# Performance work log

Hardware: AMD Instinct MI355X
Metric: run time of the kernel (lower is better)

Reference implementation:

```python
import jax, jax.numpy as jnp
import numpy as np

N_NODES = 100000


def sage_conv(x, src, dst, w_self, w_neigh, b):
    # DGL SAGEConv with 'mean' aggregator: out = x @ W_self + mean_neigh(x) @ W_neigh + b
    msg = x[src]                                                     # [E, d] gather
    agg = jax.ops.segment_sum(msg, dst, num_segments=N_NODES)        # [N, d]
    deg = jax.ops.segment_sum(jnp.ones((src.shape[0],), x.dtype), dst,
                              num_segments=N_NODES)                  # [N]
    h_neigh = agg / jnp.maximum(deg, 1.0)[:, None]                   # mean; 0 for isolated nodes
    return x @ w_self + h_neigh @ w_neigh + b


def setup_inputs() -> dict:
    key = jax.random.key(0)
    ks = jax.random.split(key, 12)
    N, E = N_NODES, 1600000
    in_f, h_f, r_f = 128, 128, 64
    glorot = lambda k, i, o: jax.random.normal(k, (i, o), jnp.float32) / np.float32(np.sqrt(i))
    return {
        "in_feat": jax.random.normal(ks[0], (N, in_f), jnp.float32),
        "src": jax.random.randint(ks[1], (E,), 0, N),
        "dst": jax.random.randint(ks[2], (E,), 0, N),
        "w1_self": glorot(ks[3], in_f, h_f), "w1_neigh": glorot(ks[4], in_f, h_f), "b1": jnp.zeros((h_f,), jnp.float32),
        "w2_self": glorot(ks[5], h_f, r_f), "w2_neigh": glorot(ks[6], h_f, r_f), "b2": jnp.zeros((r_f,), jnp.float32),
        "w3_self": glorot(ks[7], r_f, r_f), "w3_neigh": glorot(ks[8], r_f, r_f), "b3": jnp.zeros((r_f,), jnp.float32),
    }


def reference(in_feat, src, dst,
              w1_self, w1_neigh, b1,
              w2_self, w2_neigh, b2,
              w3_self, w3_neigh, b3):
    h = sage_conv(in_feat, src, dst, w1_self, w1_neigh, b1)
    h = jax.nn.relu(h)
    h = sage_conv(h, src, dst, w2_self, w2_neigh, b2)
    h = jax.nn.relu(h)
    # dropout is treated as identity (deterministic eval-mode reference)
    h = sage_conv(h, src, dst, w3_self, w3_neigh, b3)
    return jax.nn.softmax(h, axis=-1)
```

## Files before the change

kernel.cpp:

```cpp
#include <hip/hip_runtime.h>
#include <hip/hip_bf16.h>

#define N_NODES 100000

typedef unsigned short ushort_t;
typedef __attribute__((ext_vector_type(8))) short short8;
typedef __attribute__((ext_vector_type(4))) float f32x4;

static __device__ __forceinline__ ushort_t f2bf(float f) {
    unsigned u = __float_as_uint(f);
    unsigned r = u + 0x7FFFu + ((u >> 16) & 1u);
    return (ushort_t)(r >> 16);
}
static __device__ __forceinline__ float bf2f(ushort_t h) {
    return __uint_as_float(((unsigned)h) << 16);
}

static __device__ __forceinline__ void split8(const float* __restrict__ xp,
                                              short8& hi, short8& lo) {
    float4 x0 = *(const float4*)xp;
    float4 x1 = *(const float4*)(xp + 4);
    float xs[8] = {x0.x, x0.y, x0.z, x0.w, x1.x, x1.y, x1.z, x1.w};
    #pragma unroll
    for (int j = 0; j < 8; ++j) {
        ushort_t h = f2bf(xs[j]);
        hi[j] = (short)h;
        lo[j] = (short)f2bf(xs[j] - bf2f(h));
    }
}

static __device__ __forceinline__ void acc_u32(unsigned w, float& a0, float& a1) {
    a0 += __uint_as_float(w << 16);
    a1 += __uint_as_float(w & 0xFFFF0000u);
}

__global__ __launch_bounds__(256) void hist_kernel(const int* __restrict__ dst,
                                                   int* __restrict__ deg, int E) {
    int e = blockIdx.x * 256 + threadIdx.x;
    if (e < E) atomicAdd(&deg[__builtin_nontemporal_load(&dst[e])], 1);
}

__global__ __launch_bounds__(256) void scan_partial_sums(const int* __restrict__ deg,
                                                         int* __restrict__ partials, int N) {
    __shared__ int wsums[4];
    int tid = threadIdx.x, lane = tid & 63, wv = tid >> 6;
    int i0 = blockIdx.x * 1024 + tid * 4;
    int s = 0;
    #pragma unroll
    for (int j = 0; j < 4; ++j) {
        int i = i0 + j;
        if (i < N) s += deg[i];
    }
    #pragma unroll
    for (int off = 32; off > 0; off >>= 1) s += __shfl_xor(s, off, 64);
    if (lane == 0) wsums[wv] = s;
    __syncthreads();
    if (tid == 0)
        partials[blockIdx.x] = wsums[0] + wsums[1] + wsums[2] + wsums[3];
}

__global__ __launch_bounds__(256) void scan_partials(int* __restrict__ partials, int NB,
                                                     int* __restrict__ row_ptr, int N) {
    __shared__ int wsums[4];
    int tid = threadIdx.x, lane = tid & 63, wv = tid >> 6;
    int v = (tid < NB) ? partials[tid] : 0;
    int x = v;
    #pragma unroll
    for (int off = 1; off < 64; off <<= 1) {
        int y = __shfl_up(x, off, 64);
        if (lane >= off) x += y;
    }
    if (lane == 63) wsums[wv] = x;
    __syncthreads();
    int woff = 0;
    for (int w = 0; w < wv; ++w) woff += wsums[w];
    int incl = x + woff;
    if (tid < NB) partials[tid] = incl - v;
    if (tid == NB - 1) row_ptr[N] = incl;
}

__global__ __launch_bounds__(256) void scan_emit(const int* __restrict__ deg,
                                                 const int* __restrict__ partials,
                                                 int* __restrict__ row_ptr,
                                                 int* __restrict__ cursor,
                                                 float* __restrict__ inv_deg,
                                                 int* __restrict__ gcur, int N) {
    __shared__ int wsums[4];
    int tid = threadIdx.x, lane = tid & 63, wv = tid >> 6;
    int i0 = blockIdx.x * 1024 + tid * 4;
    int d[4];
    #pragma unroll
    for (int j = 0; j < 4; ++j) {
        int i = i0 + j;
        d[j] = (i < N) ? deg[i] : 0;
    }
    int s = d[0] + d[1] + d[2] + d[3];
    int x = s;
    #pragma unroll
    for (int off = 1; off < 64; off <<= 1) {
        int y = __shfl_up(x, off, 64);
        if (lane >= off) x += y;
    }
    if (lane == 63) wsums[wv] = x;
    __syncthreads();
    int woff = 0;
    for (int w = 0; w < wv; ++w) woff += wsums[w];
    int run = partials[blockIdx.x] + woff + x - s;
    #pragma unroll
    for (int j = 0; j < 4; ++j) {
        int i = i0 + j;
        if (i < N) {
            row_ptr[i] = run;
            cursor[i]  = run;
            inv_deg[i] = 1.0f / (float)(d[j] > 0 ? d[j] : 1);
            if ((i & 255) == 0) gcur[i >> 8] = run;
            run += d[j];
        }
    }
}

#define MAXBUCK 512
__global__ __launch_bounds__(256) void bin_pairs(const int* __restrict__ src,
                                                 const int* __restrict__ dst,
                                                 int* __restrict__ gcur,
                                                 long long* __restrict__ staged,
                                                 int E, int NBUCK, int C) {
    __shared__ int cnt[MAXBUCK];
    int tid = threadIdx.x;
    int e0 = blockIdx.x * C;
    int e1 = min(e0 + C, E);
    for (int b = tid; b < NBUCK; b += 256) cnt[b] = 0;
    __syncthreads();
    for (int e = e0 + tid; e < e1; e += 256) {
        int d = __builtin_nontemporal_load(&dst[e]);
        atomicAdd(&cnt[d >> 8], 1);
    }
    __syncthreads();
    for (int b = tid; b < NBUCK; b += 256) {
        int c = cnt[b];
        cnt[b] = (c > 0) ? atomicAdd(&gcur[b], c) : 0;
    }
    __syncthreads();
    for (int e = e0 + tid; e < e1; e += 256) {
        int d = __builtin_nontemporal_load(&dst[e]);
        int s = __builtin_nontemporal_load(&src[e]);
        int p = atomicAdd(&cnt[d >> 8], 1);
        staged[p] = ((long long)d << 32) | (unsigned)s;
    }
}

__global__ __launch_bounds__(256) void scatter_bucket(const long long* __restrict__ staged,
                                                      const int* __restrict__ row_ptr,
                                                      int* __restrict__ cursor,
                                                      int* __restrict__ edge_src,
                                                      int N) {
    int b = blockIdx.x;
    int lo = b << 8;
    int hiN = min((b + 1) << 8, N);
    int gstart = row_ptr[lo];
    int gend   = row_ptr[hiN];
    for (int p = gstart + threadIdx.x; p < gend; p += 256) {
        long long pr = __builtin_nontemporal_load(&staged[p]);
        int d = (int)(pr >> 32);
        int s = (int)(pr & 0xFFFFFFFFll);
        int pos = atomicAdd(&cursor[d], 1);
        edge_src[pos] = s;
    }
}

__global__ __launch_bounds__(256) void pack_all(
        const float* __restrict__ W0, const float* __restrict__ W1,
        const float* __restrict__ W2, const float* __restrict__ W3,
        const float* __restrict__ W4, const float* __restrict__ W5,
        ushort_t* H0, ushort_t* L0, ushort_t* H1, ushort_t* L1,
        ushort_t* H2, ushort_t* L2, ushort_t* H3, ushort_t* L3,
        ushort_t* H4, ushort_t* L4, ushort_t* H5, ushort_t* L5) {
    int b = blockIdx.x;
    const float* W; ushort_t* Hi; ushort_t* Lo; int K, NS, base;
    if (b < 8)       { W = W0; Hi = H0; Lo = L0; K = 128; NS = 128; base = 0;  }
    else if (b < 16) { W = W1; Hi = H1; Lo = L1; K = 128; NS = 128; base = 8;  }
    else if (b < 20) { W = W2; Hi = H2; Lo = L2; K = 128; NS = 64;  base = 16; }
    else if (b < 24) { W = W3; Hi = H3; Lo = L3; K = 128; NS = 64;  base = 20; }
    else if (b < 26) { W = W4; Hi = H4; Lo = L4; K = 64;  NS = 64;  base = 24; }
    else             { W = W5; Hi = H5; Lo = L5; K = 64;  NS = 64;  base = 26; }
    int tid = (b - base) * 256 + threadIdx.x;
    if (tid >= (K * NS) / 8) return;
    int l  = tid & 63;
    int fl = tid >> 6;
    int NT = NS / 16;
    int t = fl % NT, s = fl / NT;
    ushort_t hs[8], ls[8];
    #pragma unroll
    for (int j = 0; j < 8; ++j) {
        int k = s * 32 + (l >> 4) * 8 + j;
        int n = t * 16 + (l & 15);
        float w = W[(size_t)k * NS + n];
        ushort_t h = f2bf(w);
        hs[j] = h;
        ls[j] = f2bf(w - bf2f(h));
    }
    #pragma unroll
    for (int j = 0; j < 8; ++j) {
        Hi[(size_t)tid * 8 + j] = hs[j];
        Lo[(size_t)tid * 8 + j] = ls[j];
    }
}

template <int K, int NS>
__global__ __launch_bounds__(256) void mfma_gemm(const float* __restrict__ X,
                                                 const ushort_t* __restrict__ BsHi,
                                                 const ushort_t* __restrict__ BsLo,
                                                 const ushort_t* __restrict__ BnHi,
                                                 const ushort_t* __restrict__ BnLo,
                                                 const float* __restrict__ bias,
                                                 float* __restrict__ S,
                                                 ushort_t* __restrict__ Zb,
                                                 int M) {
    constexpr int KS = K / 32;
    constexpr int NT = NS / 16;
    __shared__ float ldsS[4][32 * 20];
    __shared__ float ldsZ[4][32 * 20];
    int tid = threadIdx.x;
    int lane = tid & 63, w = tid >> 6;
    int baseM = blockIdx.x * 128 + w * 32;
    int rIn = lane & 15, q = lane >> 4;
    float* bufS = ldsS[w];
    float* bufZ = ldsZ[w];

    short8 Ahi[KS][2], Alo[KS][2];
    #pragma unroll
    for (int s = 0; s < KS; ++s) {
        #pragma unroll
        for (int mt = 0; mt < 2; ++mt) {
            int gm = baseM + mt * 16 + rIn;
            if (gm < M) {
                split8(&X[(size_t)gm * K + s * 32 + q * 8], Ahi[s][mt], Alo[s][mt]);
            } else {
                #pragma unroll
                for (int j = 0; j < 8; ++j) { Ahi[s][mt][j] = 0; Alo[s][mt][j] = 0; }
            }
        }
    }

    for (int t = 0; t < NT; ++t) {
        f32x4 aS0 = {0.f, 0.f, 0.f, 0.f}, aS1 = {0.f, 0.f, 0.f, 0.f};
        f32x4 aZ0 = {0.f, 0.f, 0.f, 0.f}, aZ1 = {0.f, 0.f, 0.f, 0.f};
        #pragma unroll
        for (int s = 0; s < KS; ++s) {
            size_t fo = ((size_t)(s * NT + t) * 64 + lane) * 8;
            short8 bsh = *(const short8*)&BsHi[fo];
            short8 bsl = *(const short8*)&BsLo[fo];
            short8 bnh = *(const short8*)&BnHi[fo];
            short8 bnl = *(const short8*)&BnLo[fo];
            aS0 = __builtin_amdgcn_mfma_f32_16x16x32_bf16(Ahi[s][0], bsh, aS0, 0, 0, 0);
            aS0 = __builtin_amdgcn_mfma_f32_16x16x32_bf16(Alo[s][0], bsh, aS0, 0, 0, 0);
            aS0 = __builtin_amdgcn_mfma_f32_16x16x32_bf16(Ahi[s][0], bsl, aS0, 0, 0, 0);
            aS1 = __builtin_amdgcn_mfma_f32_16x16x32_bf16(Ahi[s][1], bsh, aS1, 0, 0, 0);
            aS1 = __builtin_amdgcn_mfma_f32_16x16x32_bf16(Alo[s][1], bsh, aS1, 0, 0, 0);
            aS1 = __builtin_amdgcn_mfma_f32_16x16x32_bf16(Ahi[s][1], bsl, aS1, 0, 0, 0);
            aZ0 = __builtin_amdgcn_mfma_f32_16x16x32_bf16(Ahi[s][0], bnh, aZ0, 0, 0, 0);
            aZ0 = __builtin_amdgcn_mfma_f32_16x16x32_bf16(Alo[s][0], bnh, aZ0, 0, 0, 0);
            aZ0 = __builtin_amdgcn_mfma_f32_16x16x32_bf16(Ahi[s][0], bnl, aZ0, 0, 0, 0);
            aZ1 = __builtin_amdgcn_mfma_f32_16x16x32_bf16(Ahi[s][1], bnh, aZ1, 0, 0, 0);
            aZ1 = __builtin_amdgcn_mfma_f32_16x16x32_bf16(Alo[s][1], bnh, aZ1, 0, 0, 0);
            aZ1 = __builtin_amdgcn_mfma_f32_16x16x32_bf16(Ahi[s][1], bnl, aZ1, 0, 0, 0);
        }
        #pragma unroll
        for (int r = 0; r < 4; ++r) {
            bufS[(q * 4 + r) * 20 + rIn]        = aS0[r];
            bufS[(16 + q * 4 + r) * 20 + rIn]   = aS1[r];
            bufZ[(q * 4 + r) * 20 + rIn]        = aZ0[r];
            bufZ[(16 + q * 4 + r) * 20 + rIn]   = aZ1[r];
        }
        int row = lane >> 2;
        int cq  = lane & 3;
        int col = t * 16 + cq * 4;
        float4 bv = *(const float4*)&bias[col];
        #pragma unroll
        for (int half = 0; half < 2; ++half) {
            int gm = baseM + half * 16 + row;
            float4 v = *(float4*)&bufS[(half * 16 + row) * 20 + cq * 4];
            float4 z = *(float4*)&bufZ[(half * 16 + row) * 20 + cq * 4];
            if (gm < M) {
                float4 o;
                o.x = v.x + bv.x; o.y = v.y + bv.y;
                o.z = v.z + bv.z; o.w = v.w + bv.w;
                *(float4*)&S[(size_t)gm * NS + col] = o;
                uint2 o2;
                o2.x = (unsigned)f2bf(z.x) | ((unsigned)f2bf(z.y) << 16);
                o2.y = (unsigned)f2bf(z.z) | ((unsigned)f2bf(z.w) << 16);
                *(uint2*)&Zb[(size_t)gm * NS + col] = o2;
            }
        }
    }
}

template <int D, int ACT>
__global__ __launch_bounds__(256) void agg_kernel(const float* __restrict__ S,
                                                  const ushort_t* __restrict__ Zb,
                                                  const int* __restrict__ row_ptr,
                                                  const int* __restrict__ edge_src,
                                                  const float* __restrict__ inv_deg,
                                                  float* __restrict__ out, int N) {
    constexpr int G  = 16;
    constexpr int PF = D / G;
    constexpr int NV = PF / 4;
    constexpr int NG = 256 / G;
    constexpr int U  = 8;
    int tid = threadIdx.x;
    int g = tid >> 4, fl = tid & 15;
    int n = blockIdx.x * NG + g;
    if (n >= N) return;
    int beg = row_ptr[n], end = row_ptr[n + 1];

    float acc[2][PF];
    #pragma unroll
    for (int i = 0; i < PF; ++i) { acc[0][i] = 0.f; acc[1][i] = 0.f; }

    const char* zlane = (const char*)Zb + fl * (PF * 2);

    for (int j = beg; j < end; j += U) {
        int srcs[U];
        #pragma unroll
        for (int k = 0; k < U; ++k)
            srcs[k] = (j + k < end) ? __builtin_nontemporal_load(&edge_src[j + k]) : -1;

        if constexpr (PF == 8) {
            uint4 u[U];
            #pragma unroll
            for (int k = 0; k < U; ++k) {
                u[k] = make_uint4(0u, 0u, 0u, 0u);
                if (srcs[k] >= 0)
                    u[k] = *(const uint4*)(zlane + ((size_t)((unsigned)srcs[k]) << 8));
            }
            #pragma unroll
            for (int k = 0; k < U; ++k) {
                acc_u32(u[k].x, acc[k & 1][0], acc[k & 1][1]);
                acc_u32(u[k].y, acc[k & 1][2], acc[k & 1][3]);
                acc_u32(u[k].z, acc[k & 1][4], acc[k & 1][5]);
                acc_u32(u[k].w, acc[k & 1][6], acc[k & 1][7]);
            }
        } else {
            uint2 u[U];
            #pragma unroll
            for (int k = 0; k < U; ++k) {
                u[k] = make_uint2(0u, 0u);
                if (srcs[k] >= 0)
                    u[k] = *(const uint2*)(zlane + ((size_t)((unsigned)srcs[k]) << 7));
            }
            #pragma unroll
            for (int k = 0; k < U; ++k) {
                acc_u32(u[k].x, acc[k & 1][0], acc[k & 1][1]);
                acc_u32(u[k].y, acc[k & 1][2], acc[k & 1][3]);
            }
        }
    }

    float id = inv_deg[n];
    const f32x4* Sp = (const f32x4*)(S + (size_t)n * D) + fl * NV;
    float4*      Op = (float4*)(out + (size_t)n * D) + fl * NV;
    float v[PF];
    #pragma unroll
    for (int q = 0; q < NV; ++q) {
        f32x4 s4 = __builtin_nontemporal_load(Sp + q);
        v[q * 4 + 0] = s4[0] + id * (acc[0][q * 4 + 0] + acc[1][q * 4 + 0]);
        v[q * 4 + 1] = s4[1] + id * (acc[0][q * 4 + 1] + acc[1][q * 4 + 1]);
        v[q * 4 + 2] = s4[2] + id * (acc[0][q * 4 + 2] + acc[1][q * 4 + 2]);
        v[q * 4 + 3] = s4[3] + id * (acc[0][q * 4 + 3] + acc[1][q * 4 + 3]);
    }

    if constexpr (ACT == 0) {
        #pragma unroll
        for (int q = 0; q < NV; ++q) {
            float4 o;
            o.x = fmaxf(v[q * 4 + 0], 0.f);
            o.y = fmaxf(v[q * 4 + 1], 0.f);
            o.z = fmaxf(v[q * 4 + 2], 0.f);
            o.w = fmaxf(v[q * 4 + 3], 0.f);
            Op[q] = o;
        }
    } else {
        float m = fmaxf(fmaxf(v[0], v[1]), fmaxf(v[2], v[3]));
        #pragma unroll
        for (int off = 8; off > 0; off >>= 1) m = fmaxf(m, __shfl_xor(m, off, 16));
        float e0 = __expf(v[0] - m), e1 = __expf(v[1] - m);
        float e2 = __expf(v[2] - m), e3 = __expf(v[3] - m);
        float s = (e0 + e1) + (e2 + e3);
        #pragma unroll
        for (int off = 8; off > 0; off >>= 1) s += __shfl_xor(s, off, 16);
        float inv = 1.0f / s;
        float4 o;
        o.x = e0 * inv; o.y = e1 * inv; o.z = e2 * inv; o.w = e3 * inv;
        Op[0] = o;
    }
}

extern "C" void kernel_launch(void* const* d_in, const int* in_sizes, int n_in,
                              void* d_out, int out_size, void* d_ws, size_t ws_size,
                              hipStream_t stream) {
    const float* in_feat = (const float*)d_in[0];
    const int*   src     = (const int*)d_in[1];
    const int*   dst     = (const int*)d_in[2];
    const float* w1s = (const float*)d_in[3];
    const float* w1n = (const float*)d_in[4];
    const float* b1  = (const float*)d_in[5];
    const float* w2s = (const float*)d_in[6];
    const float* w2n = (const float*)d_in[7];
    const float* b2  = (const float*)d_in[8];
    const float* w3s = (const float*)d_in[9];
    const float* w3n = (const float*)d_in[10];
    const float* b3  = (const float*)d_in[11];

    const int N = N_NODES;
    const int E = in_sizes[1];

    char* p = (char*)d_ws;
    auto carve = [&](size_t bytes) -> char* {
        char* q = p;
        p += (bytes + 511) & ~(size_t)511;
        return q;
    };
    float*    S        = (float*)   carve((size_t)N * 128 * sizeof(float));
    ushort_t* Zb       = (ushort_t*)carve((size_t)N * 128 * sizeof(ushort_t));
    float*    H        = (float*)   carve((size_t)N * 128 * sizeof(float));
    int*      edge_src = (int*)     carve((size_t)E * sizeof(int));
    int*      row_ptr  = (int*)     carve((size_t)(N + 1) * sizeof(int));
    int*      cursor   = (int*)     carve((size_t)N * sizeof(int));
    int*      deg      = (int*)     carve((size_t)N * sizeof(int));
    float*    invd     = (float*)   carve((size_t)N * sizeof(float));
    int*      partials = (int*)     carve(256 * sizeof(int));
    int*      gcur     = (int*)     carve(MAXBUCK * sizeof(int));
    long long* staged  = (long long*)H;
    ushort_t* P1sH = (ushort_t*)carve(128 * 128 * 2); ushort_t* P1sL = (ushort_t*)carve(128 * 128 * 2);
    ushort_t* P1nH = (ushort_t*)carve(128 * 128 * 2); ushort_t* P1nL = (ushort_t*)carve(128 * 128 * 2);
    ushort_t* P2sH = (ushort_t*)carve(128 * 64 * 2);  ushort_t* P2sL = (ushort_t*)carve(128 * 64 * 2);
    ushort_t* P2nH = (ushort_t*)carve(128 * 64 * 2);  ushort_t* P2nL = (ushort_t*)carve(128 * 64 * 2);
    ushort_t* P3sH = (ushort_t*)carve(64 * 64 * 2);   ushort_t* P3sL = (ushort_t*)carve(64 * 64 * 2);
    ushort_t* P3nH = (ushort_t*)carve(64 * 64 * 2);   ushort_t* P3nL = (ushort_t*)carve(64 * 64 * 2);

    pack_all<<<28, 256, 0, stream>>>(w1s, w1n, w2s, w2n, w3s, w3n,
                                     P1sH, P1sL, P1nH, P1nL,
                                     P2sH, P2sL, P2nH, P2nL,
                                     P3sH, P3sL, P3nH, P3nL);

    (void)hipMemsetAsync(deg, 0, (size_t)N * sizeof(int), stream);
    hist_kernel<<<(E + 255) / 256, 256, 0, stream>>>(dst, deg, E);
    const int NB = (N + 1023) / 1024;
    scan_partial_sums<<<NB, 256, 0, stream>>>(deg, partials, N);
    scan_partials<<<1, 256, 0, stream>>>(partials, NB, row_ptr, N);
    scan_emit<<<NB, 256, 0, stream>>>(deg, partials, row_ptr, cursor, invd, gcur, N);
    const int NBUCK = (N + 255) >> 8;
    const int BINB  = 256;
    const int CHUNK = (E + BINB - 1) / BINB;
    bin_pairs<<<BINB, 256, 0, stream>>>(src, dst, gcur, staged, E, NBUCK, CHUNK);
    scatter_bucket<<<NBUCK, 256, 0, stream>>>(staged, row_ptr, cursor, edge_src, N);

    const int GB = (N + 127) / 128;
    const int AB = (N + 15) / 16;

    mfma_gemm<128, 128><<<GB, 256, 0, stream>>>(in_feat, P1sH, P1sL, P1nH, P1nL, b1, S, Zb, N);
    agg_kernel<128, 0><<<AB, 256, 0, stream>>>(S, Zb, row_ptr, edge_src, invd, H, N);

    mfma_gemm<128, 64><<<GB, 256, 0, stream>>>(H, P2sH, P2sL, P2nH, P2nL, b2, S, Zb, N);
    agg_kernel<64, 0><<<AB, 256, 0, stream>>>(S, Zb, row_ptr, edge_src, invd, H, N);

    mfma_gemm<64, 64><<<GB, 256, 0, stream>>>(H, P3sH, P3sL, P3nH, P3nL, b3, S, Zb, N);
    agg_kernel<64, 1><<<AB, 256, 0, stream>>>(S, Zb, row_ptr, edge_src, invd,
                                              (float*)d_out, N);
}
```

Measured before the change: 476.6 us.

## Resize aggregation lane groups per feature width and fuse weight pack with histogram

```diff
diff --git a/kernel.cpp b/kernel.cpp
--- a/kernel.cpp
+++ b/kernel.cpp
@@ -34,11 +34,6 @@
     a1 += __uint_as_float(w & 0xFFFF0000u);
 }
 
-__global__ __launch_bounds__(256) void hist_kernel(const int* __restrict__ dst,
-                                                   int* __restrict__ deg, int E) {
-    int e = blockIdx.x * 256 + threadIdx.x;
-    if (e < E) atomicAdd(&deg[__builtin_nontemporal_load(&dst[e])], 1);
-}
 
 __global__ __launch_bounds__(256) void scan_partial_sums(const int* __restrict__ deg,
                                                          int* __restrict__ partials, int N) {
@@ -168,14 +163,20 @@
     }
 }
 
-__global__ __launch_bounds__(256) void pack_all(
+__global__ __launch_bounds__(256) void pack_hist(
         const float* __restrict__ W0, const float* __restrict__ W1,
         const float* __restrict__ W2, const float* __restrict__ W3,
         const float* __restrict__ W4, const float* __restrict__ W5,
         ushort_t* H0, ushort_t* L0, ushort_t* H1, ushort_t* L1,
         ushort_t* H2, ushort_t* L2, ushort_t* H3, ushort_t* L3,
-        ushort_t* H4, ushort_t* L4, ushort_t* H5, ushort_t* L5) {
+        ushort_t* H4, ushort_t* L4, ushort_t* H5, ushort_t* L5,
+        const int* __restrict__ dst, int* __restrict__ deg, int E) {
     int b = blockIdx.x;
+    if (b >= 28) {
+        int e = (b - 28) * 256 + threadIdx.x;
+        if (e < E) atomicAdd(&deg[__builtin_nontemporal_load(&dst[e])], 1);
+        return;
+    }
     const float* W; ushort_t* Hi; ushort_t* Lo; int K, NS, base;
     if (b < 8)       { W = W0; Hi = H0; Lo = L0; K = 128; NS = 128; base = 0;  }
     else if (b < 16) { W = W1; Hi = H1; Lo = L1; K = 128; NS = 128; base = 8;  }
@@ -302,96 +303,78 @@
                                                   const int* __restrict__ edge_src,
                                                   const float* __restrict__ inv_deg,
                                                   float* __restrict__ out, int N) {
-    constexpr int G  = 16;
-    constexpr int PF = D / G;
-    constexpr int NV = PF / 4;
+    constexpr int G  = D / 8;
+    constexpr int PF = 8;
     constexpr int NG = 256 / G;
-    constexpr int U  = 8;
+    constexpr int U  = G;
     int tid = threadIdx.x;
-    int g = tid >> 4, fl = tid & 15;
+    int g = tid / G, fl = tid % G;
     int n = blockIdx.x * NG + g;
     if (n >= N) return;
     int beg = row_ptr[n], end = row_ptr[n + 1];
+    float id = inv_deg[n];
+
+    const f32x4* Sp = (const f32x4*)(S + (size_t)n * D) + fl * 2;
+    f32x4 s40 = __builtin_nontemporal_load(Sp);
+    f32x4 s41 = __builtin_nontemporal_load(Sp + 1);
 
     float acc[2][PF];
     #pragma unroll
     for (int i = 0; i < PF; ++i) { acc[0][i] = 0.f; acc[1][i] = 0.f; }
 
-    const char* zlane = (const char*)Zb + fl * (PF * 2);
+    const char* zlane = (const char*)Zb + fl * 16;
 
     for (int j = beg; j < end; j += U) {
-        int srcs[U];
-        #pragma unroll
-        for (int k = 0; k < U; ++k)
-            srcs[k] = (j + k < end) ? __builtin_nontemporal_load(&edge_src[j + k]) : -1;
-
-        if constexpr (PF == 8) {
-            uint4 u[U];
-            #pragma unroll
-            for (int k = 0; k < U; ++k) {
-                u[k] = make_uint4(0u, 0u, 0u, 0u);
-                if (srcs[k] >= 0)
-                    u[k] = *(const uint4*)(zlane + ((size_t)((unsigned)srcs[k]) << 8));
-            }
-            #pragma unroll
-            for (int k = 0; k < U; ++k) {
-                acc_u32(u[k].x, acc[k & 1][0], acc[k & 1][1]);
-                acc_u32(u[k].y, acc[k & 1][2], acc[k & 1][3]);
-                acc_u32(u[k].z, acc[k & 1][4], acc[k & 1][5]);
-                acc_u32(u[k].w, acc[k & 1][6], acc[k & 1][7]);
-            }
-        } else {
-            uint2 u[U];
-            #pragma unroll
-            for (int k = 0; k < U; ++k) {
-                u[k] = make_uint2(0u, 0u);
-                if (srcs[k] >= 0)
-                    u[k] = *(const uint2*)(zlane + ((size_t)((unsigned)srcs[k]) << 7));
-            }
-            #pragma unroll
-            for (int k = 0; k < U; ++k) {
-                acc_u32(u[k].x, acc[k & 1][0], acc[k & 1][1]);
-                acc_u32(u[k].y, acc[k & 1][2], acc[k & 1][3]);
-            }
-        }
-    }
-
-    float id = inv_deg[n];
-    const f32x4* Sp = (const f32x4*)(S + (size_t)n * D) + fl * NV;
-    float4*      Op = (float4*)(out + (size_t)n * D) + fl * NV;
+        int je = j + fl;
+        int myS = (je < end) ? __builtin_nontemporal_load(&edge_src[je]) : -1;
+        uint4 u[U];
+        #pragma unroll
+        for (int k = 0; k < U; ++k) {
+            int s = __shfl(myS, k, U);
+            u[k] = make_uint4(0u, 0u, 0u, 0u);
+            if (s >= 0)
+                u[k] = *(const uint4*)(zlane + ((size_t)((unsigned)s) * (D * 2)));
+        }
+        #pragma unroll
+        for (int k = 0; k < U; ++k) {
+            acc_u32(u[k].x, acc[k & 1][0], acc[k & 1][1]);
+            acc_u32(u[k].y, acc[k & 1][2], acc[k & 1][3]);
+            acc_u32(u[k].z, acc[k & 1][4], acc[k & 1][5]);
+            acc_u32(u[k].w, acc[k & 1][6], acc[k & 1][7]);
+        }
+    }
+
     float v[PF];
     #pragma unroll
-    for (int q = 0; q < NV; ++q) {
-        f32x4 s4 = __builtin_nontemporal_load(Sp + q);
-        v[q * 4 + 0] = s4[0] + id * (acc[0][q * 4 + 0] + acc[1][q * 4 + 0]);
-        v[q * 4 + 1] = s4[1] + id * (acc[0][q * 4 + 1] + acc[1][q * 4 + 1]);
-        v[q * 4 + 2] = s4[2] + id * (acc[0][q * 4 + 2] + acc[1][q * 4 + 2]);
-        v[q * 4 + 3] = s4[3] + id * (acc[0][q * 4 + 3] + acc[1][q * 4 + 3]);
-    }
-
+    for (int i = 0; i < 4; ++i) {
+        v[i]     = s40[i] + id * (acc[0][i]     + acc[1][i]);
+        v[4 + i] = s41[i] + id * (acc[0][4 + i] + acc[1][4 + i]);
+    }
+
+    float4* Op = (float4*)(out + (size_t)n * D) + fl * 2;
     if constexpr (ACT == 0) {
-        #pragma unroll
-        for (int q = 0; q < NV; ++q) {
-            float4 o;
-            o.x = fmaxf(v[q * 4 + 0], 0.f);
-            o.y = fmaxf(v[q * 4 + 1], 0.f);
-            o.z = fmaxf(v[q * 4 + 2], 0.f);
-            o.w = fmaxf(v[q * 4 + 3], 0.f);
-            Op[q] = o;
-        }
+        float4 o0, o1;
+        o0.x = fmaxf(v[0], 0.f); o0.y = fmaxf(v[1], 0.f);
+        o0.z = fmaxf(v[2], 0.f); o0.w = fmaxf(v[3], 0.f);
+        o1.x = fmaxf(v[4], 0.f); o1.y = fmaxf(v[5], 0.f);
+        o1.z = fmaxf(v[6], 0.f); o1.w = fmaxf(v[7], 0.f);
+        Op[0] = o0; Op[1] = o1;
     } else {
-        float m = fmaxf(fmaxf(v[0], v[1]), fmaxf(v[2], v[3]));
-        #pragma unroll
-        for (int off = 8; off > 0; off >>= 1) m = fmaxf(m, __shfl_xor(m, off, 16));
-        float e0 = __expf(v[0] - m), e1 = __expf(v[1] - m);
-        float e2 = __expf(v[2] - m), e3 = __expf(v[3] - m);
-        float s = (e0 + e1) + (e2 + e3);
-        #pragma unroll
-        for (int off = 8; off > 0; off >>= 1) s += __shfl_xor(s, off, 16);
+        float m = v[0];
+        #pragma unroll
+        for (int i = 1; i < 8; ++i) m = fmaxf(m, v[i]);
+        #pragma unroll
+        for (int off = 4; off > 0; off >>= 1) m = fmaxf(m, __shfl_xor(m, off, 8));
+        float e[8], s = 0.f;
+        #pragma unroll
+        for (int i = 0; i < 8; ++i) { e[i] = __expf(v[i] - m); s += e[i]; }
+        #pragma unroll
+        for (int off = 4; off > 0; off >>= 1) s += __shfl_xor(s, off, 8);
         float inv = 1.0f / s;
-        float4 o;
-        o.x = e0 * inv; o.y = e1 * inv; o.z = e2 * inv; o.w = e3 * inv;
-        Op[0] = o;
+        float4 o0, o1;
+        o0.x = e[0] * inv; o0.y = e[1] * inv; o0.z = e[2] * inv; o0.w = e[3] * inv;
+        o1.x = e[4] * inv; o1.y = e[5] * inv; o1.z = e[6] * inv; o1.w = e[7] * inv;
+        Op[0] = o0; Op[1] = o1;
     }
 }
 
@@ -438,13 +421,13 @@
     ushort_t* P3sH = (ushort_t*)carve(64 * 64 * 2);   ushort_t* P3sL = (ushort_t*)carve(64 * 64 * 2);
     ushort_t* P3nH = (ushort_t*)carve(64 * 64 * 2);   ushort_t* P3nL = (ushort_t*)carve(64 * 64 * 2);
 
-    pack_all<<<28, 256, 0, stream>>>(w1s, w1n, w2s, w2n, w3s, w3n,
-                                     P1sH, P1sL, P1nH, P1nL,
-                                     P2sH, P2sL, P2nH, P2nL,
-                                     P3sH, P3sL, P3nH, P3nL);
-
     (void)hipMemsetAsync(deg, 0, (size_t)N * sizeof(int), stream);
-    hist_kernel<<<(E + 255) / 256, 256, 0, stream>>>(dst, deg, E);
+    pack_hist<<<28 + (E + 255) / 256, 256, 0, stream>>>(
+        w1s, w1n, w2s, w2n, w3s, w3n,
+        P1sH, P1sL, P1nH, P1nL,
+        P2sH, P2sL, P2nH, P2nL,
+        P3sH, P3sL, P3nH, P3nL,
+        dst, deg, E);
     const int NB = (N + 1023) / 1024;
     scan_partial_sums<<<NB, 256, 0, stream>>>(deg, partials, N);
     scan_partials<<<1, 256, 0, stream>>>(partials, NB, row_ptr, N);
@@ -455,16 +438,17 @@
     bin_pairs<<<BINB, 256, 0, stream>>>(src, dst, gcur, staged, E, NBUCK, CHUNK);
     scatter_bucket<<<NBUCK, 256, 0, stream>>>(staged, row_ptr, cursor, edge_src, N);
 
-    const int GB = (N + 127) / 128;
-    const int AB = (N + 15) / 16;
+    const int GB   = (N + 127) / 128;
+    const int AB128 = (N + 15) / 16;
+    const int AB64  = (N + 31) / 32;
 
     mfma_gemm<128, 128><<<GB, 256, 0, stream>>>(in_feat, P1sH, P1sL, P1nH, P1nL, b1, S, Zb, N);
-    agg_kernel<128, 0><<<AB, 256, 0, stream>>>(S, Zb, row_ptr, edge_src, invd, H, N);
+    agg_kernel<128, 0><<<AB128, 256, 0, stream>>>(S, Zb, row_ptr, edge_src, invd, H, N);
 
     mfma_gemm<128, 64><<<GB, 256, 0, stream>>>(H, P2sH, P2sL, P2nH, P2nL, b2, S, Zb, N);
-    agg_kernel<64, 0><<<AB, 256, 0, stream>>>(S, Zb, row_ptr, edge_src, invd, H, N);
+    agg_kernel<64, 0><<<AB64, 256, 0, stream>>>(S, Zb, row_ptr, edge_src, invd, H, N);
 
     mfma_gemm<64, 64><<<GB, 256, 0, stream>>>(H, P3sH, P3sL, P3nH, P3nL, b3, S, Zb, N);
-    agg_kernel<64, 1><<<AB, 256, 0, stream>>>(S, Zb, row_ptr, edge_src, invd,
-                                              (float*)d_out, N);
-}
+    agg_kernel<64, 1><<<AB64, 256, 0, stream>>>(S, Zb, row_ptr, edge_src, invd,
+                                                (float*)d_out, N);
+}
```

Result: faster. 465.8 us, median of 2 (-2.3%).
